# Optimization experiments

Measured on AMD Instinct MI355X. Metric: run time of the kernel, lower is better.

Reference implementation:

```python
import jax, jax.numpy as jnp
import numpy as np

DIM = 256
DEPTH = 6
HEADS = 8
DH = DIM // HEADS            # 32
BUCKET = 64
TEMP = 0.75                  # sort-net softmax temperature
FF = 4 * DIM
B, T = 4, 8192


def layernorm(x, g, b, eps=1e-5):
    m = x.mean(-1, keepdims=True)
    v = ((x - m) ** 2).mean(-1, keepdims=True)
    return (x - m) * jax.lax.rsqrt(v + eps) * g + b


def sinkhorn_attn(q, k, v):
    # q,k,v: (bh, t, dh). Bucketed attention with differentiable top-1 bucket routing
    bh, t, dh = q.shape
    nb = t // BUCKET
    bq = q.reshape(bh, nb, BUCKET, dh)
    bk = k.reshape(bh, nb, BUCKET, dh)
    bv = v.reshape(bh, nb, BUCKET, dh)
    # sort net: bucket summaries -> routing matrix R (differentiable_topk, k=1)
    sq = bq.mean(2)                                   # (bh, nb, dh)
    sk = bk.mean(2)
    R = jnp.einsum('bie,bje->bij', sq, sk) * (dh ** -0.5)
    probs = jax.nn.softmax(R / TEMP, axis=-1)
    top = jnp.max(probs, axis=-1, keepdims=True)      # (bh, nb, 1)
    idx = jnp.argmax(probs, axis=-1)                  # (bh, nb)
    Rtop = jax.nn.one_hot(idx, nb, dtype=q.dtype) * top
    # gather routed key/value buckets (weighted by routing prob)
    bk_r = jnp.einsum('bij,bjtd->bitd', Rtop, bk)
    bv_r = jnp.einsum('bij,bjtd->bitd', Rtop, bv)
    K = jnp.concatenate([bk_r, bk], axis=2)           # (bh, nb, 2*BUCKET, dh)
    V = jnp.concatenate([bv_r, bv], axis=2)
    dots = jnp.einsum('buie,buje->buij', bq, K) * (dh ** -0.5)
    attn = jax.nn.softmax(dots, axis=-1)
    out = jnp.einsum('buij,buje->buie', attn, V)
    return out.reshape(bh, t, dh)


def setup_inputs() -> dict:
    key = jax.random.key(0)
    ks = jax.random.split(key, 18)
    s = 0.02
    f32 = jnp.float32
    inp = {
        'x': jax.random.normal(ks[0], (B, DIM, T), f32),
        'pe0': jax.random.normal(ks[1], (T // BUCKET, DIM), f32) * s,
        'pe1': jax.random.normal(ks[2], (BUCKET, DIM), f32) * s,
        'ln1_g': jnp.ones((DEPTH, DIM), f32),
        'ln1_b': jnp.zeros((DEPTH, DIM), f32),
        'Wq': jax.random.normal(ks[3], (DEPTH, DIM, DIM), f32) * s,
        'Wkv': jax.random.normal(ks[4], (DEPTH, DIM, 2 * DIM), f32) * s,
        'Wo': jax.random.normal(ks[5], (DEPTH, DIM, DIM), f32) * s,
        'bo': jnp.zeros((DEPTH, DIM), f32),
        'ln2_g': jnp.ones((DEPTH, DIM), f32),
        'ln2_b': jnp.zeros((DEPTH, DIM), f32),
        'W1': jax.random.normal(ks[6], (DEPTH, DIM, FF), f32) * s,
        'b1': jnp.zeros((DEPTH, FF), f32),
        'W2': jax.random.normal(ks[7], (DEPTH, FF, DIM), f32) * s,
        'b2': jnp.zeros((DEPTH, DIM), f32),
        'gf': jnp.ones((DIM,), f32),
        'bf': jnp.zeros((DIM,), f32),
    }
    return inp


def _forward(x, pe0, pe1, ln1_g, ln1_b, Wq, Wkv, Wo, bo, ln2_g, ln2_b, W1, b1, W2, b2, gf, bf):
    b, _, t = x.shape
    y = jnp.transpose(x, (0, 2, 1))                      # (b, t, dim)
    pos = (pe0[:, None, :] + pe1[None, :, :]).reshape(-1, DIM)[:t]
    y = y + pos

    def split_heads(u):
        return u.reshape(b, t, HEADS, DH).transpose(0, 2, 1, 3).reshape(b * HEADS, t, DH)

    def step(y, p):
        g1, b1_, wq, wkv, wo, bo_, g2, b2_, w1, bb1, w2, bb2 = p
        h = layernorm(y, g1, b1_)
        q = h @ wq
        k, v = jnp.split(h @ wkv, 2, axis=-1)
        o = sinkhorn_attn(split_heads(q), split_heads(k), split_heads(v))
        o = o.reshape(b, HEADS, t, DH).transpose(0, 2, 1, 3).reshape(b, t, DIM)
        y = y + o @ wo + bo_
        h = layernorm(y, g2, b2_)
        y = y + jax.nn.gelu(h @ w1 + bb1, approximate=False) @ w2 + bb2
        return y, None

    y, _ = jax.lax.scan(step, y, (ln1_g, ln1_b, Wq, Wkv, Wo, bo, ln2_g, ln2_b, W1, b1, W2, b2))
    y = layernorm(y, gf, bf)
    return jnp.transpose(y, (0, 2, 1))


def reference(x, pe0, pe1, ln1_g, ln1_b, Wq, Wkv, Wo, bo, ln2_g, ln2_b, W1, b1, W2, b2, gf, bf):
    return _forward(x, pe0, pe1, ln1_g, ln1_b, Wq, Wkv, Wo, bo, ln2_g, ln2_b, W1, b1, W2, b2, gf, bf)
```

## Files before the change

kernel.cpp:

```cpp
#include <hip/hip_runtime.h>
#include <cstdint>
#include <cstddef>

#define T_LEN 8192
#define DIMC  256
#define NBUCK 128
#define BHEAD 32
#define MROWS 32768

typedef __attribute__((ext_vector_type(8))) short bf16x8;
typedef __attribute__((ext_vector_type(4))) float f32x4;

__device__ __forceinline__ ushort f2bf(float x) {
  union { float f; unsigned u; } v; v.f = x;
  unsigned r = v.u + 0x7fffu + ((v.u >> 16) & 1u);
  return (ushort)(r >> 16);
}
__device__ __forceinline__ float bf2f(ushort u) {
  union { unsigned u; float f; } v; v.u = ((unsigned)u) << 16; return v.f;
}

__device__ __forceinline__ void gld16(const void* g, void* l) {
  __builtin_amdgcn_global_load_lds((const __attribute__((address_space(1))) void*)g,
                                   (__attribute__((address_space(3))) void*)l, 16, 0, 0);
}

__device__ __forceinline__ float fast_gelu(float v) {
  float x = v * 0.70710678118654752f;
  float ax = fabsf(x);
  float t = 1.0f / fmaf(0.3275911f, ax, 1.0f);
  float poly = t * fmaf(t, fmaf(t, fmaf(t, fmaf(t, 1.061405429f, -1.453152027f),
                                        1.421413741f), -0.284496736f), 0.254829592f);
  float e = __expf(-ax * ax);
  float er = 1.0f - poly * e;
  er = (x < 0.f) ? -er : er;
  return 0.5f * v * (1.0f + er);
}

__global__ __launch_bounds__(256)
void add_pos_k(const float* __restrict__ x, const float* __restrict__ pe0,
               const float* __restrict__ pe1, float* __restrict__ y) {
  __shared__ float tile[32][33];
  int b  = blockIdx.z;
  int t0 = blockIdx.x * 32;
  int d0 = blockIdx.y * 32;
  int tj = threadIdx.x;
  int di = threadIdx.y;
#pragma unroll
  for (int k = 0; k < 4; k++) {
    int d = d0 + di + k * 8;
    tile[di + k * 8][tj] = x[((size_t)b * DIMC + d) * T_LEN + t0 + tj];
  }
  __syncthreads();
#pragma unroll
  for (int k = 0; k < 4; k++) {
    int t = t0 + di + k * 8;
    int d = d0 + tj;
    y[((size_t)b * T_LEN + t) * DIMC + d] =
        tile[tj][di + k * 8] + pe0[(size_t)(t >> 6) * DIMC + d] + pe1[(size_t)(t & 63) * DIMC + d];
  }
}

__global__ __launch_bounds__(256)
void layernorm_k(const float* __restrict__ x, const float* __restrict__ g,
                 const float* __restrict__ b, ushort* __restrict__ o) {
  int row  = blockIdx.x * 4 + (threadIdx.x >> 6);
  int lane = threadIdx.x & 63;
  const float4* xr = (const float4*)(x + (size_t)row * DIMC);
  float4 v = xr[lane];
  float s  = v.x + v.y + v.z + v.w;
  float s2 = v.x * v.x + v.y * v.y + v.z * v.z + v.w * v.w;
#pragma unroll
  for (int off = 32; off; off >>= 1) {
    s  += __shfl_xor(s, off);
    s2 += __shfl_xor(s2, off);
  }
  float mean = s * (1.0f / 256.0f);
  float var  = s2 * (1.0f / 256.0f) - mean * mean;
  float r    = rsqrtf(var + 1e-5f);
  float4 gv = ((const float4*)g)[lane];
  float4 bv = ((const float4*)b)[lane];
  ushort4 o4;
  o4.x = f2bf((v.x - mean) * r * gv.x + bv.x);
  o4.y = f2bf((v.y - mean) * r * gv.y + bv.y);
  o4.z = f2bf((v.z - mean) * r * gv.z + bv.z);
  o4.w = f2bf((v.w - mean) * r * gv.w + bv.w);
  ((ushort4*)(o + (size_t)row * DIMC))[lane] = o4;
}

__global__ __launch_bounds__(256)
void wt_bf16_k(const float* __restrict__ W, ushort* __restrict__ Wt,
               int K, int N, size_t outStride) {
  __shared__ float t[32][33];
  int l = blockIdx.z;
  const float* Wl = W + (size_t)l * K * N;
  ushort* Wtl = Wt + (size_t)l * outStride;
  int n0 = blockIdx.x * 32, k0 = blockIdx.y * 32;
  int tx = threadIdx.x, ty = threadIdx.y;
#pragma unroll
  for (int p = 0; p < 4; p++)
    t[ty + p * 8][tx] = Wl[(size_t)(k0 + ty + p * 8) * N + n0 + tx];
  __syncthreads();
#pragma unroll
  for (int p = 0; p < 4; p++)
    Wtl[(size_t)(n0 + ty + p * 8) * K + k0 + tx] = f2bf(t[tx][ty + p * 8]);
}

template <int EPI>
__global__ __launch_bounds__(256)
void gemm_bf16(const ushort* __restrict__ A, const ushort* __restrict__ Bt,
               const float* __restrict__ bias, ushort* __restrict__ Cbf,
               int N, int K, int lda, int ldb) {
  __shared__ ushort As[128 * 32];
  __shared__ ushort Bs[128 * 32];
  __shared__ ushort eb[4][16][66];
  int tid = threadIdx.x;
  int w = tid >> 6, lane = tid & 63;
  int bm = blockIdx.x << 7, bn = blockIdx.y << 7;
  int wm = (w >> 1) << 6, wn = (w & 1) << 6;
  int l15 = lane & 15, quad = lane >> 4;

  int off0 = (w << 11) + (lane << 4);
  int off1 = off0 + 1024;
  int r0 = off0 >> 6, c0 = (off0 & 63) >> 1;
  int r1 = off1 >> 6, c1 = (off1 & 63) >> 1;
  const ushort* ga0 = A + (size_t)(bm + r0) * lda + c0;
  const ushort* ga1 = A + (size_t)(bm + r1) * lda + c1;
  const ushort* gb0 = Bt + (size_t)(bn + r0) * ldb + c0;
  const ushort* gb1 = Bt + (size_t)(bn + r1) * ldb + c1;
  ushort* lA0 = As + (w << 10);
  ushort* lA1 = lA0 + 512;
  ushort* lB0 = Bs + (w << 10);
  ushort* lB1 = lB0 + 512;

  f32x4 acc[4][4];
#pragma unroll
  for (int i = 0; i < 4; i++)
#pragma unroll
    for (int j = 0; j < 4; j++) {
      f32x4 z = {0.f, 0.f, 0.f, 0.f};
      acc[i][j] = z;
    }

  for (int k0 = 0; k0 < K; k0 += 32) {
    gld16(ga0 + k0, lA0);
    gld16(ga1 + k0, lA1);
    gld16(gb0 + k0, lB0);
    gld16(gb1 + k0, lB1);
    __syncthreads();
    bf16x8 aF[4], bF[4];
#pragma unroll
    for (int i = 0; i < 4; i++)
      aF[i] = *(const bf16x8*)(As + ((wm + (i << 4) + l15) << 5) + (quad << 3));
#pragma unroll
    for (int j = 0; j < 4; j++)
      bF[j] = *(const bf16x8*)(Bs + ((wn + (j << 4) + l15) << 5) + (quad << 3));
#pragma unroll
    for (int i = 0; i < 4; i++)
#pragma unroll
      for (int j = 0; j < 4; j++)
        acc[i][j] = __builtin_amdgcn_mfma_f32_16x16x32_bf16(aF[i], bF[j], acc[i][j], 0, 0, 0);
    __syncthreads();
  }

  float bvj[4];
  if (EPI == 1) {
#pragma unroll
    for (int j = 0; j < 4; j++) bvj[j] = bias[bn + wn + (j << 4) + l15];
  }
#pragma unroll
  for (int i = 0; i < 4; i++) {
#pragma unroll
    for (int j = 0; j < 4; j++) {
#pragma unroll
      for (int r = 0; r < 4; r++) {
        float v = acc[i][j][r];
        if (EPI == 1) v = fast_gelu(v + bvj[j]);
        eb[w][(quad << 2) + r][(j << 4) + l15] = f2bf(v);
      }
    }
#pragma unroll
    for (int h = 0; h < 2; h++) {
      int chunk = (h << 6) + lane;
      int row = chunk >> 3, c8 = (chunk & 7) << 3;
      bf16x8 vv = *(const bf16x8*)&eb[w][row][c8];
      *(bf16x8*)&Cbf[(size_t)(bm + wm + (i << 4) + row) * N + bn + wn + c8] = vv;
    }
  }
}

template <int FINAL>
__global__ __launch_bounds__(256)
void oproj_ln_k(const ushort* __restrict__ A, const ushort* __restrict__ Bt,
                const float* __restrict__ bias, float* __restrict__ y,
                const float* __restrict__ g, const float* __restrict__ b,
                ushort* __restrict__ obf, int K, int lda) {
  __shared__ ushort smem[64 * 264];
  __shared__ float red[2][64][2];
  __shared__ float stat[64][2];
  ushort* As = smem;
  ushort* Bs = smem + 2048;
  int tid = threadIdx.x;
  int wid = tid >> 6, lane = tid & 63;
  int l15 = lane & 15, quad = lane >> 4;
  int bm = blockIdx.x << 6;
  int wm = (wid >> 1) << 5;
  int wn = (wid & 1) << 7;

  const ushort* gaA = A + (size_t)(bm + (tid >> 2)) * lda + ((tid & 3) << 3);
  ushort* lA = As + (tid << 3);
  const ushort* gaB[4];
  ushort* lB[4];
#pragma unroll
  for (int p = 0; p < 4; p++) {
    int u = (p << 8) + tid;
    gaB[p] = Bt + (size_t)(u >> 2) * K + ((u & 3) << 3);
    lB[p] = Bs + (u << 3);
  }

  f32x4 acc[2][8];
#pragma unroll
  for (int i = 0; i < 2; i++)
#pragma unroll
    for (int j = 0; j < 8; j++) {
      f32x4 z = {0.f, 0.f, 0.f, 0.f};
      acc[i][j] = z;
    }

  for (int k0 = 0; k0 < K; k0 += 32) {
    gld16(gaA + k0, lA);
#pragma unroll
    for (int p = 0; p < 4; p++) gld16(gaB[p] + k0, lB[p]);
    __syncthreads();
    bf16x8 aF[2];
#pragma unroll
    for (int i = 0; i < 2; i++)
      aF[i] = *(const bf16x8*)(As + ((wm + (i << 4) + l15) << 5) + (quad << 3));
#pragma unroll
    for (int j = 0; j < 8; j++) {
      bf16x8 bF = *(const bf16x8*)(Bs + ((wn + (j << 4) + l15) << 5) + (quad << 3));
#pragma unroll
      for (int i = 0; i < 2; i++)
        acc[i][j] = __builtin_amdgcn_mfma_f32_16x16x32_bf16(aF[i], bF, acc[i][j], 0, 0, 0);
    }
    __syncthreads();
  }

  float bc[8];
#pragma unroll
  for (int j = 0; j < 8; j++) bc[j] = bias[wn + (j << 4) + l15];
  float s1v[2][4], s2v[2][4];
#pragma unroll
  for (int i = 0; i < 2; i++)
#pragma unroll
    for (int r = 0; r < 4; r++) {
      int row = bm + wm + (i << 4) + (quad << 2) + r;
      float s1 = 0.f, s2 = 0.f;
#pragma unroll
      for (int j = 0; j < 8; j++) {
        size_t idx = (size_t)row * 256 + wn + (j << 4) + l15;
        float v = acc[i][j][r] + bc[j] + y[idx];
        acc[i][j][r] = v;
        if (!FINAL) y[idx] = v;
        s1 += v;
        s2 += v * v;
      }
      s1v[i][r] = s1;
      s2v[i][r] = s2;
    }
#pragma unroll
  for (int off = 1; off < 16; off <<= 1)
#pragma unroll
    for (int i = 0; i < 2; i++)
#pragma unroll
      for (int r = 0; r < 4; r++) {
        s1v[i][r] += __shfl_xor(s1v[i][r], off);
        s2v[i][r] += __shfl_xor(s2v[i][r], off);
      }
  if (l15 == 0) {
#pragma unroll
    for (int i = 0; i < 2; i++)
#pragma unroll
      for (int r = 0; r < 4; r++) {
        int lr = wm + (i << 4) + (quad << 2) + r;
        red[wid & 1][lr][0] = s1v[i][r];
        red[wid & 1][lr][1] = s2v[i][r];
      }
  }
  __syncthreads();
  if (tid < 64) {
    float s  = red[0][tid][0] + red[1][tid][0];
    float s2 = red[0][tid][1] + red[1][tid][1];
    float mean = s * (1.0f / 256.0f);
    float var  = s2 * (1.0f / 256.0f) - mean * mean;
    stat[tid][0] = mean;
    stat[tid][1] = rsqrtf(var + 1e-5f);
  }
  __syncthreads();

  if (FINAL) {
#pragma unroll
    for (int j = 0; j < 8; j++) {
      int col = wn + (j << 4) + l15;
      float gc = g[col], bc2 = b[col];
#pragma unroll
      for (int i = 0; i < 2; i++)
#pragma unroll
        for (int r = 0; r < 4; r++) {
          int lr = wm + (i << 4) + (quad << 2) + r;
          float o = (acc[i][j][r] - stat[lr][0]) * stat[lr][1] * gc + bc2;
          y[(size_t)(bm + lr) * 256 + col] = o;
        }
    }
  } else {
    ushort (*eb)[264] = (ushort(*)[264])smem;
#pragma unroll
    for (int j = 0; j < 8; j++) {
      int col = wn + (j << 4) + l15;
      float gc = g[col], bc2 = b[col];
#pragma unroll
      for (int i = 0; i < 2; i++)
#pragma unroll
        for (int r = 0; r < 4; r++) {
          int lr = wm + (i << 4) + (quad << 2) + r;
          float o = (acc[i][j][r] - stat[lr][0]) * stat[lr][1] * gc + bc2;
          eb[lr][col] = f2bf(o);
        }
    }
    __syncthreads();
#pragma unroll
    for (int h = 0; h < 8; h++) {
      int chunk = (h << 8) + tid;
      int row = chunk >> 5, c8 = (chunk & 31) << 3;
      bf16x8 vv = *(const bf16x8*)&eb[row][c8];
      *(bf16x8*)&obf[(size_t)(bm + row) * 256 + c8] = vv;
    }
  }
}

__global__ __launch_bounds__(64)
void summary_k(const ushort* __restrict__ qkv,
               float* __restrict__ sq, float* __restrict__ sk) {
  int blk = blockIdx.x;
  int bh = blk >> 7, ib = blk & 127;
  int b = bh >> 3, h = bh & 7;
  int lane = threadIdx.x;
  int d = lane & 31;
  bool isK = lane >= 32;
  size_t base = ((size_t)b * T_LEN + (size_t)ib * 64) * 768 + (isK ? 256 : 0) + h * 32 + d;
  float s = 0.f;
#pragma unroll 8
  for (int t = 0; t < 64; t++) s += bf2f(qkv[base + (size_t)t * 768]);
  s *= (1.0f / 64.0f);
  float* dst = isK ? sk : sq;
  dst[((size_t)bh * NBUCK + ib) * 32 + d] = s;
}

__global__ __launch_bounds__(64)
void route_k(const float* __restrict__ sq, const float* __restrict__ sk,
             int* __restrict__ ridx, float* __restrict__ rw) {
  int blk = blockIdx.x;
  int bh = blk >> 7, ib = blk & 127;
  int lane = threadIdx.x;
  const float* qrow = sq + ((size_t)bh * NBUCK + ib) * 32;
  const float* k0 = sk + ((size_t)bh * NBUCK + lane) * 32;
  const float* k1 = k0 + 64 * 32;
  float s0 = 0.f, s1 = 0.f;
#pragma unroll
  for (int d = 0; d < 32; d++) {
    float qd = qrow[d];
    s0 += qd * k0[d];
    s1 += qd * k1[d];
  }
  const float sc = 0.17677669529663687f * (4.0f / 3.0f);
  float L0 = s0 * sc, L1 = s1 * sc;
  float m = fmaxf(L0, L1);
#pragma unroll
  for (int off = 32; off; off >>= 1) m = fmaxf(m, __shfl_xor(m, off));
  float Z = expf(L0 - m) + expf(L1 - m);
#pragma unroll
  for (int off = 32; off; off >>= 1) Z += __shfl_xor(Z, off);
  float mv = (L1 > L0) ? L1 : L0;
  int mj = (L1 > L0) ? lane + 64 : lane;
#pragma unroll
  for (int off = 32; off; off >>= 1) {
    float ov = __shfl_xor(mv, off);
    int oj = __shfl_xor(mj, off);
    if (ov > mv || (ov == mv && oj < mj)) { mv = ov; mj = oj; }
  }
  if (lane == 0) {
    ridx[blk] = mj;
    rw[blk] = 1.0f / Z;
  }
}

__global__ __launch_bounds__(256)
void attn_mfma_k(const ushort* __restrict__ qkv,
                 const int* __restrict__ ridx, const float* __restrict__ rw,
                 ushort* __restrict__ o) {
  __shared__ ushort Qs[64][40];
  __shared__ ushort Ks[128][40];
  __shared__ ushort Vt[32][136];
  __shared__ ushort Ps[4][16][136];
  int blk = blockIdx.x;
  int bh = blk >> 7, ib = blk & 127;
  int b = bh >> 3, h = bh & 7;
  int tid = threadIdx.x;
  int jr = ridx[blk];
  float w = rw[blk];
  {
    int r = tid >> 2, c = (tid & 3) << 3;
    const ushort* src = qkv + ((size_t)b * T_LEN + (size_t)ib * 64 + r) * 768 + h * 32 + c;
    *(bf16x8*)&Qs[r][c] = *(const bf16x8*)src;
  }
#pragma unroll
  for (int p = 0; p < 2; p++) {
    int idx = tid + (p << 8);
    int r = idx >> 2, c = (idx & 3) << 3;
    int srcb = (r < 64) ? jr : ib;
    int tt = r & 63;
    const ushort* src = qkv + ((size_t)b * T_LEN + (size_t)srcb * 64 + tt) * 768 + 256 + h * 32 + c;
    *(bf16x8*)&Ks[r][c] = *(const bf16x8*)src;
  }
  {
    int tok = tid >> 1, d0 = (tid & 1) << 4;
    int srcb = (tok < 64) ? jr : ib;
    int tt = tok & 63;
    const ushort* src = qkv + ((size_t)b * T_LEN + (size_t)srcb * 64 + tt) * 768 + 512 + h * 32 + d0;
    bf16x8 v0 = *(const bf16x8*)src;
    bf16x8 v1 = *(const bf16x8*)(src + 8);
#pragma unroll
    for (int j = 0; j < 8; j++) {
      Vt[d0 + j][tok] = (ushort)v0[j];
      Vt[d0 + 8 + j][tok] = (ushort)v1[j];
    }
  }
  __syncthreads();
  int wid = tid >> 6, lane = tid & 63, l15 = lane & 15, quad = lane >> 4;
  bf16x8 aQ = *(const bf16x8*)&Qs[(wid << 4) + l15][quad << 3];
  f32x4 sf[8];
#pragma unroll
  for (int jn = 0; jn < 8; jn++) {
    bf16x8 bK = *(const bf16x8*)&Ks[(jn << 4) + l15][quad << 3];
    f32x4 z = {0.f, 0.f, 0.f, 0.f};
    sf[jn] = __builtin_amdgcn_mfma_f32_16x16x32_bf16(aQ, bK, z, 0, 0, 0);
  }
  const float sc = 0.17677669529663687f;
#pragma unroll
  for (int jn = 0; jn < 8; jn++) {
    float mult = (jn < 4) ? w * sc : sc;
#pragma unroll
    for (int r = 0; r < 4; r++) sf[jn][r] *= mult;
  }
  float mx[4], sm[4], inv[4];
#pragma unroll
  for (int r = 0; r < 4; r++) {
    float m = sf[0][r];
#pragma unroll
    for (int jn = 1; jn < 8; jn++) m = fmaxf(m, sf[jn][r]);
    mx[r] = m;
  }
#pragma unroll
  for (int off = 1; off < 16; off <<= 1)
#pragma unroll
    for (int r = 0; r < 4; r++) mx[r] = fmaxf(mx[r], __shfl_xor(mx[r], off));
#pragma unroll
  for (int r = 0; r < 4; r++) sm[r] = 0.f;
#pragma unroll
  for (int jn = 0; jn < 8; jn++)
#pragma unroll
    for (int r = 0; r < 4; r++) {
      sf[jn][r] = expf(sf[jn][r] - mx[r]);
      sm[r] += sf[jn][r];
    }
#pragma unroll
  for (int off = 1; off < 16; off <<= 1)
#pragma unroll
    for (int r = 0; r < 4; r++) sm[r] += __shfl_xor(sm[r], off);
#pragma unroll
  for (int r = 0; r < 4; r++) inv[r] = 1.0f / sm[r];
#pragma unroll
  for (int jn = 0; jn < 8; jn++) {
    float ws2 = (jn < 4) ? w : 1.f;
#pragma unroll
    for (int r = 0; r < 4; r++)
      Ps[wid][(quad << 2) + r][(jn << 4) + l15] = f2bf(sf[jn][r] * inv[r] * ws2);
  }
  f32x4 of[2];
#pragma unroll
  for (int nd = 0; nd < 2; nd++) { f32x4 z = {0.f, 0.f, 0.f, 0.f}; of[nd] = z; }
#pragma unroll
  for (int kk = 0; kk < 4; kk++) {
    bf16x8 aP = *(const bf16x8*)&Ps[wid][l15][(kk << 5) + (quad << 3)];
#pragma unroll
    for (int nd = 0; nd < 2; nd++) {
      bf16x8 bV = *(const bf16x8*)&Vt[(nd << 4) + l15][(kk << 5) + (quad << 3)];
      of[nd] = __builtin_amdgcn_mfma_f32_16x16x32_bf16(aP, bV, of[nd], 0, 0, 0);
    }
  }
  ushort* obase = o + ((size_t)b * T_LEN + (size_t)ib * 64 + (wid << 4) + (quad << 2)) * 256 + h * 32 + l15;
#pragma unroll
  for (int nd = 0; nd < 2; nd++)
#pragma unroll
    for (int r = 0; r < 4; r++)
      obase[(size_t)r * 256 + (nd << 4)] = f2bf(of[nd][r]);
}

__global__ __launch_bounds__(256)
void transpose_out_k(const float* __restrict__ yln, float* __restrict__ out) {
  __shared__ float tile[32][33];
  int b  = blockIdx.z;
  int t0 = blockIdx.x * 32;
  int d0 = blockIdx.y * 32;
  int tx = threadIdx.x;
  int ty = threadIdx.y;
#pragma unroll
  for (int k = 0; k < 4; k++) {
    int t = t0 + ty + k * 8;
    tile[ty + k * 8][tx] = yln[((size_t)b * T_LEN + t) * DIMC + d0 + tx];
  }
  __syncthreads();
#pragma unroll
  for (int k = 0; k < 4; k++) {
    int d = d0 + ty + k * 8;
    out[((size_t)b * DIMC + d) * T_LEN + t0 + tx] = tile[tx][ty + k * 8];
  }
}

extern "C" void kernel_launch(void* const* d_in, const int* in_sizes, int n_in,
                              void* d_out, int out_size, void* d_ws, size_t ws_size,
                              hipStream_t stream) {
  const float* x     = (const float*)d_in[0];
  const float* pe0   = (const float*)d_in[1];
  const float* pe1   = (const float*)d_in[2];
  const float* ln1_g = (const float*)d_in[3];
  const float* ln1_b = (const float*)d_in[4];
  const float* Wq    = (const float*)d_in[5];
  const float* Wkv   = (const float*)d_in[6];
  const float* Wo    = (const float*)d_in[7];
  const float* bo    = (const float*)d_in[8];
  const float* ln2_g = (const float*)d_in[9];
  const float* ln2_b = (const float*)d_in[10];
  const float* W1    = (const float*)d_in[11];
  const float* b1    = (const float*)d_in[12];
  const float* W2    = (const float*)d_in[13];
  const float* b2    = (const float*)d_in[14];
  const float* gf    = (const float*)d_in[15];
  const float* bfp   = (const float*)d_in[16];
  float* out = (float*)d_out;

  const int M = MROWS;
  float*  y    = (float*)d_ws;
  ushort* qkv  = (ushort*)(y + (size_t)M * 256);
  ushort* bufA = qkv + (size_t)M * 768;
  ushort* bufB = bufA + (size_t)M * 256;
  ushort* wbf  = bufB + (size_t)M * 256;
  float*  sqb  = (float*)(wbf + (size_t)6 * 786432);
  float*  skb  = sqb + 131072;
  float*  rwb  = skb + 131072;
  int*    rib  = (int*)(rwb + 4096);
  ushort* ffbf = qkv;

  dim3 tb(32, 8);
  wt_bf16_k<<<dim3(8, 8, 6),  tb, 0, stream>>>(Wq,  wbf + 0,      256, 256,  786432);
  wt_bf16_k<<<dim3(16, 8, 6), tb, 0, stream>>>(Wkv, wbf + 65536,  256, 512,  786432);
  wt_bf16_k<<<dim3(8, 8, 6),  tb, 0, stream>>>(Wo,  wbf + 196608, 256, 256,  786432);
  wt_bf16_k<<<dim3(32, 8, 6), tb, 0, stream>>>(W1,  wbf + 262144, 256, 1024, 786432);
  wt_bf16_k<<<dim3(8, 32, 6), tb, 0, stream>>>(W2,  wbf + 524288, 1024, 256, 786432);

  add_pos_k<<<dim3(T_LEN / 32, DIMC / 32, 4), tb, 0, stream>>>(x, pe0, pe1, y);
  layernorm_k<<<M / 4, 256, 0, stream>>>(y, ln1_g, ln1_b, bufB);

  for (int l = 0; l < 6; l++) {
    const ushort* wl    = wbf + (size_t)l * 786432;
    const ushort* wqkvT = wl;
    const ushort* woT   = wl + 196608;
    const ushort* w1T   = wl + 262144;
    const ushort* w2T   = wl + 524288;

    gemm_bf16<0><<<dim3(M / 128, 6), 256, 0, stream>>>(bufB, wqkvT, nullptr, qkv, 768, 256, 256, 256);
    summary_k<<<BHEAD * NBUCK, 64, 0, stream>>>(qkv, sqb, skb);
    route_k<<<BHEAD * NBUCK, 64, 0, stream>>>(sqb, skb, rib, rwb);
    attn_mfma_k<<<BHEAD * NBUCK, 256, 0, stream>>>(qkv, rib, rwb, bufA);
    oproj_ln_k<0><<<M / 64, 256, 0, stream>>>(bufA, woT, bo + l * 256, y,
                                              ln2_g + l * 256, ln2_b + l * 256,
                                              bufB, 256, 256);
    gemm_bf16<1><<<dim3(M / 128, 8), 256, 0, stream>>>(bufB, w1T, b1 + l * 1024, ffbf, 1024, 256, 256, 256);
    if (l < 5) {
      oproj_ln_k<0><<<M / 64, 256, 0, stream>>>(ffbf, w2T, b2 + l * 256, y,
                                                ln1_g + (l + 1) * 256, ln1_b + (l + 1) * 256,
                                                bufB, 1024, 1024);
    } else {
      oproj_ln_k<1><<<M / 64, 256, 0, stream>>>(ffbf, w2T, b2 + l * 256, y,
                                                gf, bfp, nullptr, 1024, 1024);
    }
  }

  transpose_out_k<<<dim3(T_LEN / 32, DIMC / 32, 4), tb, 0, stream>>>(y, out);

  (void)in_sizes; (void)n_in; (void)out_size; (void)ws_size;
}
```

Baseline: 1.256 ms.

## Swizzle LDS tiles in GEMMs, use tanh GELU and fast softmax intrinsics

After: 1.167 ms. -7.1%, faster.

```diff
diff --git a/kernel.cpp b/kernel.cpp
--- a/kernel.cpp
+++ b/kernel.cpp
@@ -26,15 +26,10 @@
 }
 
 __device__ __forceinline__ float fast_gelu(float v) {
-  float x = v * 0.70710678118654752f;
-  float ax = fabsf(x);
-  float t = 1.0f / fmaf(0.3275911f, ax, 1.0f);
-  float poly = t * fmaf(t, fmaf(t, fmaf(t, fmaf(t, 1.061405429f, -1.453152027f),
-                                        1.421413741f), -0.284496736f), 0.254829592f);
-  float e = __expf(-ax * ax);
-  float er = 1.0f - poly * e;
-  er = (x < 0.f) ? -er : er;
-  return 0.5f * v * (1.0f + er);
+  float t2 = fmaf(v * v, 0.07135481283f, 1.5957691216f);
+  float z  = v * t2;
+  float e  = __expf(-z);
+  return v * __builtin_amdgcn_rcpf(1.0f + e);
 }
 
 __global__ __launch_bounds__(256)
@@ -122,16 +117,19 @@
 
   int off0 = (w << 11) + (lane << 4);
   int off1 = off0 + 1024;
-  int r0 = off0 >> 6, c0 = (off0 & 63) >> 1;
-  int r1 = off1 >> 6, c1 = (off1 & 63) >> 1;
-  const ushort* ga0 = A + (size_t)(bm + r0) * lda + c0;
-  const ushort* ga1 = A + (size_t)(bm + r1) * lda + c1;
-  const ushort* gb0 = Bt + (size_t)(bn + r0) * ldb + c0;
-  const ushort* gb1 = Bt + (size_t)(bn + r1) * ldb + c1;
+  int r0 = off0 >> 6;
+  int r1 = off1 >> 6;
+  int swc = (((lane & 3) ^ ((lane >> 3) & 3)) << 3);
+  const ushort* ga0 = A + (size_t)(bm + r0) * lda + swc;
+  const ushort* ga1 = A + (size_t)(bm + r1) * lda + swc;
+  const ushort* gb0 = Bt + (size_t)(bn + r0) * ldb + swc;
+  const ushort* gb1 = Bt + (size_t)(bn + r1) * ldb + swc;
   ushort* lA0 = As + (w << 10);
   ushort* lA1 = lA0 + 512;
   ushort* lB0 = Bs + (w << 10);
   ushort* lB1 = lB0 + 512;
+
+  int sq = quad ^ ((l15 >> 1) & 3);
 
   f32x4 acc[4][4];
 #pragma unroll
@@ -151,10 +149,10 @@
     bf16x8 aF[4], bF[4];
 #pragma unroll
     for (int i = 0; i < 4; i++)
-      aF[i] = *(const bf16x8*)(As + ((wm + (i << 4) + l15) << 5) + (quad << 3));
+      aF[i] = *(const bf16x8*)(As + ((wm + (i << 4) + l15) << 5) + (sq << 3));
 #pragma unroll
     for (int j = 0; j < 4; j++)
-      bF[j] = *(const bf16x8*)(Bs + ((wn + (j << 4) + l15) << 5) + (quad << 3));
+      bF[j] = *(const bf16x8*)(Bs + ((wn + (j << 4) + l15) << 5) + (sq << 3));
 #pragma unroll
     for (int i = 0; i < 4; i++)
 #pragma unroll
@@ -207,16 +205,19 @@
   int wm = (wid >> 1) << 5;
   int wn = (wid & 1) << 7;
 
-  const ushort* gaA = A + (size_t)(bm + (tid >> 2)) * lda + ((tid & 3) << 3);
+  int swc = (((tid & 3) ^ ((tid >> 3) & 3)) << 3);
+  const ushort* gaA = A + (size_t)(bm + (tid >> 2)) * lda + swc;
   ushort* lA = As + (tid << 3);
   const ushort* gaB[4];
   ushort* lB[4];
 #pragma unroll
   for (int p = 0; p < 4; p++) {
     int u = (p << 8) + tid;
-    gaB[p] = Bt + (size_t)(u >> 2) * K + ((u & 3) << 3);
+    gaB[p] = Bt + (size_t)(u >> 2) * K + swc;
     lB[p] = Bs + (u << 3);
   }
+
+  int sq = quad ^ ((l15 >> 1) & 3);
 
   f32x4 acc[2][8];
 #pragma unroll
@@ -235,10 +236,10 @@
     bf16x8 aF[2];
 #pragma unroll
     for (int i = 0; i < 2; i++)
-      aF[i] = *(const bf16x8*)(As + ((wm + (i << 4) + l15) << 5) + (quad << 3));
+      aF[i] = *(const bf16x8*)(As + ((wm + (i << 4) + l15) << 5) + (sq << 3));
 #pragma unroll
     for (int j = 0; j < 8; j++) {
-      bf16x8 bF = *(const bf16x8*)(Bs + ((wn + (j << 4) + l15) << 5) + (quad << 3));
+      bf16x8 bF = *(const bf16x8*)(Bs + ((wn + (j << 4) + l15) << 5) + (sq << 3));
 #pragma unroll
       for (int i = 0; i < 2; i++)
         acc[i][j] = __builtin_amdgcn_mfma_f32_16x16x32_bf16(aF[i], bF, acc[i][j], 0, 0, 0);
@@ -470,7 +471,7 @@
   for (int jn = 0; jn < 8; jn++)
 #pragma unroll
     for (int r = 0; r < 4; r++) {
-      sf[jn][r] = expf(sf[jn][r] - mx[r]);
+      sf[jn][r] = __expf(sf[jn][r] - mx[r]);
       sm[r] += sf[jn][r];
     }
 #pragma unroll
@@ -478,7 +479,7 @@
 #pragma unroll
     for (int r = 0; r < 4; r++) sm[r] += __shfl_xor(sm[r], off);
 #pragma unroll
-  for (int r = 0; r < 4; r++) inv[r] = 1.0f / sm[r];
+  for (int r = 0; r < 4; r++) inv[r] = __builtin_amdgcn_rcpf(sm[r]);
 #pragma unroll
   for (int jn = 0; jn < 8; jn++) {
     float ws2 = (jn < 4) ? w : 1.f;
```
